# Kernel optimization log

Hardware: AMD Instinct MI355X
Metric: run time of the kernel (lower is better)

Reference implementation:

```python
import jax, jax.numpy as jnp
import numpy as np
from jax import lax

B, T, H, L, LAT, OUT, NH = 4096, 60, 512, 2, 128, 14, 4
EPS = 1e-5


def _ln(x, g, b):
    m = x.mean(-1, keepdims=True)
    v = ((x - m) ** 2).mean(-1, keepdims=True)
    return (x - m) / jnp.sqrt(v + EPS) * g + b


def setup_inputs() -> dict:
    key = jax.random.key(0)
    ks = jax.random.split(key, 24)
    f32 = jnp.float32
    def rn(k, shape, s=0.05):
        return jax.random.normal(k, shape, dtype=f32) * s
    return {
        'x': jax.random.normal(ks[0], (B, T, 17), dtype=f32),
        'conv1_w': rn(ks[1], (24, 9, 3)), 'conv1_b': rn(ks[2], (24,)),
        'bn1_g': jnp.ones(24, f32), 'bn1_b': jnp.zeros(24, f32),
        'bn1_rm': rn(ks[3], (24,), 0.1), 'bn1_rv': jnp.full((24,), 0.8, f32),
        'comp_w': rn(ks[4], (20, 8)), 'comp_b': rn(ks[5], (20,)),
        'proj_w': rn(ks[6], (H, 44)), 'proj_b': rn(ks[7], (H,)),
        'gates_w': rn(ks[8], (L, 5, H, 2 * H), 0.02), 'gates_b': rn(ks[9], (L, 5, H)),
        'retention': jnp.full((L, H), 0.9, f32),
        'expln_g': jnp.ones((L, H), f32), 'expln_b': jnp.zeros((L, H), f32),
        'ln_g': jnp.ones((L, H), f32), 'ln_b': jnp.zeros((L, H), f32),
        'attn_in_w': rn(ks[10], (3 * H, H), 0.02), 'attn_in_b': rn(ks[11], (3 * H,)),
        'attn_out_w': rn(ks[12], (H, H), 0.02), 'attn_out_b': rn(ks[13], (H,)),
        'bneck_w': rn(ks[14], (LAT, H)), 'bneck_b': rn(ks[15], (LAT,)),
        'bn2_g': jnp.ones(LAT, f32), 'bn2_b': jnp.zeros(LAT, f32),
        'bn2_rm': rn(ks[16], (LAT,), 0.1), 'bn2_rv': jnp.full((LAT,), 0.9, f32),
        'out_w': rn(ks[17], (OUT, LAT)), 'out_b': rn(ks[18], (OUT,)),
    }


def _forward(x, conv1_w, conv1_b, bn1_g, bn1_b, bn1_rm, bn1_rv, comp_w, comp_b,
             proj_w, proj_b, gates_w, gates_b, retention, expln_g, expln_b,
             ln_g, ln_b, attn_in_w, attn_in_b, attn_out_w, attn_out_b,
             bneck_w, bneck_b, bn2_g, bn2_b, bn2_rm, bn2_rv, out_w, out_b):
    bsz = x.shape[0]
    hd = proj_w.shape[0]
    nlayers = gates_w.shape[0]
    # --- conv branch on relative features (eval-mode BatchNorm) ---
    rel = x[:, :, :9].transpose(0, 2, 1)                      # [B,9,T]
    y = lax.conv_general_dilated(rel, conv1_w, (1,), [(1, 1)],
                                 dimension_numbers=('NCH', 'OIH', 'NCH'))
    y = jax.nn.relu(y + conv1_b[None, :, None])
    y = (y - bn1_rm[None, :, None]) / jnp.sqrt(bn1_rv + EPS)[None, :, None] \
        * bn1_g[None, :, None] + bn1_b[None, :, None]
    th = y.shape[2] // 2
    y = y[:, :, :th * 2].reshape(bsz, 24, th, 2).max(-1)      # MaxPool1d(2)
    rel_feat = y.transpose(0, 2, 1)                           # [B,30,24]
    # --- company embedding branch ---
    comp = jax.nn.relu(x[:, :30, 9:] @ comp_w.T + comp_b)     # [B,30,20]
    combined = jnp.concatenate([rel_feat, comp], -1) @ proj_w.T + proj_b  # [B,30,H]
    # --- stacked xLSTM over time ---
    h0 = jnp.zeros((nlayers, bsz, hd), x.dtype)
    c0 = jnp.zeros((nlayers, bsz, hd), x.dtype)
    def step(carry, x_t):
        h, c = carry
        inp = x_t
        hs, cs = [], []
        for l in range(nlayers):
            comb = jnp.concatenate([inp, h[l]], -1)           # [B,2H]
            g = jnp.einsum('bk,ghk->gbh', comb, gates_w[l]) + gates_b[l][:, None, :]
            f = jax.nn.sigmoid(g[0]); i = jax.nn.sigmoid(g[1])
            o = jax.nn.sigmoid(g[2]); cc = jnp.tanh(g[3]); m = jax.nn.sigmoid(g[4])
            r = retention[l]
            c_new = f * c[l] + i * cc
            c_new = c_new * r + (1 - r) * c[l]
            c_new = m * c_new + (1 - m) * c[l]
            o_exp = jax.nn.sigmoid(_ln(o, expln_g[l], expln_b[l]))  # exp(z)/(1+exp(z))
            h_new = _ln(o_exp * jnp.tanh(c_new), ln_g[l], ln_b[l])
            hs.append(h_new); cs.append(c_new)
            inp = h_new
        return (jnp.stack(hs), jnp.stack(cs)), inp
    _, seq = lax.scan(step, (h0, c0), combined.transpose(1, 0, 2))
    seq = seq.transpose(1, 0, 2)                              # [B,30,H]
    # --- multi-head self attention (eval, 4 heads) ---
    dh = hd // NH
    qkv = seq @ attn_in_w.T + attn_in_b
    q, k, v = jnp.split(qkv, 3, axis=-1)
    q = q.reshape(bsz, -1, NH, dh); k = k.reshape(bsz, -1, NH, dh); v = v.reshape(bsz, -1, NH, dh)
    scores = jnp.einsum('bqhd,bkhd->bhqk', q, k) / jnp.sqrt(jnp.float32(dh))
    attn = jnp.einsum('bhqk,bkhd->bqhd', jax.nn.softmax(scores, -1), v)
    attn = attn.reshape(bsz, -1, hd) @ attn_out_w.T + attn_out_b
    final = attn[:, -1, :]
    latent = final @ bneck_w.T + bneck_b
    latent = (latent - bn2_rm) / jnp.sqrt(bn2_rv + EPS) * bn2_g + bn2_b
    return latent @ out_w.T + out_b


def reference(x, conv1_w, conv1_b, bn1_g, bn1_b, bn1_rm, bn1_rv, comp_w, comp_b,
              proj_w, proj_b, gates_w, gates_b, retention, expln_g, expln_b,
              ln_g, ln_b, attn_in_w, attn_in_b, attn_out_w, attn_out_b,
              bneck_w, bneck_b, bn2_g, bn2_b, bn2_rm, bn2_rv, out_w, out_b):
    return _forward(x, conv1_w, conv1_b, bn1_g, bn1_b, bn1_rm, bn1_rv, comp_w, comp_b,
                    proj_w, proj_b, gates_w, gates_b, retention, expln_g, expln_b,
                    ln_g, ln_b, attn_in_w, attn_in_b, attn_out_w, attn_out_b,
                    bneck_w, bneck_b, bn2_g, bn2_b, bn2_rm, bn2_rv, out_w, out_b)
```

## Files before the change

kernel.cpp:

```cpp
#include <hip/hip_runtime.h>
#include <hip/hip_bf16.h>
#include <hip/hip_fp16.h>

#define B_   4096
#define T_   60
#define TT   30
#define H_   512
#define L_   2
#define NH_  4
#define DH_  128
#define LAT_ 128
#define OUT_ 14
#define NGATE_ (5*H_)
#define EPSF 1e-5f
#define FEATK 64
#define K0M  (FEATK + H_)

typedef __attribute__((ext_vector_type(8))) short bf16x8;
typedef __attribute__((ext_vector_type(4))) short sh4;
typedef __attribute__((ext_vector_type(4))) float f32x4;

__device__ __forceinline__ float sigmoidf_(float x) { return 1.0f / (1.0f + __expf(-x)); }
__device__ __forceinline__ float bf2f(short s) {
    return __uint_as_float(((unsigned)(unsigned short)s) << 16);
}

__device__ __forceinline__ void async_load16(const void* g, void* l) {
    __builtin_amdgcn_global_load_lds((const __attribute__((address_space(1))) void*)g,
                                     (__attribute__((address_space(3))) void*)l, 16, 0, 0);
}

__device__ __forceinline__ int perm_row(int n) {
    int g = n >> 9, j = n & 511;
    return (j >> 4) * 80 + g * 16 + (j & 15);
}

__global__ __launch_bounds__(256) void cvt_bf16(const float* __restrict__ in,
                                                __hip_bfloat16* __restrict__ out, long n) {
    long i = (long)blockIdx.x * blockDim.x + threadIdx.x;
    long stride = (long)gridDim.x * blockDim.x;
    for (; i < n; i += stride) out[i] = __float2bfloat16(in[i]);
}

__global__ __launch_bounds__(256) void zero_f32(float* __restrict__ p, long n) {
    long i = (long)blockIdx.x * blockDim.x + threadIdx.x;
    long stride = (long)gridDim.x * blockDim.x;
    for (; i < n; i += stride) p[i] = 0.0f;
}

__global__ __launch_bounds__(256)
void perm_w1(const float* __restrict__ gw, __hip_bfloat16* __restrict__ w1p) {
    long i = (long)blockIdx.x * 256 + threadIdx.x;
    if (i >= (long)NGATE_ * 2 * H_) return;
    int n = (int)(i >> 10), k = (int)(i & 1023);
    w1p[(long)perm_row(n) * (2 * H_) + k] = __float2bfloat16(gw[i]);
}

__global__ __launch_bounds__(256)
void build_w0m(const float* __restrict__ gw, const float* __restrict__ pw,
               const float* __restrict__ pb, const float* __restrict__ gb,
               __hip_bfloat16* __restrict__ w0p, float* __restrict__ bc) {
    const int tid = threadIdx.x;
    const int n = blockIdx.x * 4 + (tid >> 6);
    const int f = tid & 63;
    const long np = perm_row(n);
    const float* wrow = gw + (long)n * (2 * H_);
    float acc = 0.f;
    if (f < 44) {
        for (int k = 0; k < H_; ++k) acc += wrow[k] * pw[k * 44 + f];
    }
    w0p[np * K0M + f] = __float2bfloat16(acc);
    #pragma unroll
    for (int j = 0; j < 8; ++j) {
        int col = f * 8 + j;
        w0p[np * K0M + FEATK + col] = __float2bfloat16(wrow[H_ + col]);
    }
    float s = 0.f;
    #pragma unroll
    for (int j = 0; j < 8; ++j) s += wrow[f * 8 + j] * pb[f * 8 + j];
    #pragma unroll
    for (int off = 32; off > 0; off >>= 1) s += __shfl_down(s, off, 64);
    if (f == 0) bc[n] = gb[n] + s;
}

__global__ __launch_bounds__(256)
void build_wkt(const float* __restrict__ aiw, __hip_bfloat16* __restrict__ wkt) {
    int i = blockIdx.x * 256 + threadIdx.x;
    if (i >= 2048 * 128) return;
    int row = i >> 7;
    int k = i & 127;
    int h = row >> 9, j = row & 511;
    wkt[i] = __float2bfloat16(aiw[(H_ + h * 128 + k) * H_ + j]);
}

__global__ __launch_bounds__(256)
void frontend_kernel(const float* __restrict__ x,
                     const float* __restrict__ cw, const float* __restrict__ cb,
                     const float* __restrict__ bg, const float* __restrict__ bb,
                     const float* __restrict__ brm, const float* __restrict__ brv,
                     const float* __restrict__ compw, const float* __restrict__ compb,
                     __hip_bfloat16* __restrict__ feat_out) {
    const int b = blockIdx.x, tid = threadIdx.x;
    __shared__ float xs[T_ * 17];
    __shared__ float ybuf[24][T_];
    __shared__ float feat[TT][44];

    for (int i = tid; i < T_ * 17; i += 256) xs[i] = x[(long)b * T_ * 17 + i];
    __syncthreads();

    for (int i = tid; i < 24 * T_; i += 256) {
        int oc = i / T_, t = i % T_;
        float acc = cb[oc];
        #pragma unroll
        for (int kk = 0; kk < 3; ++kk) {
            int tt = t + kk - 1;
            if (tt >= 0 && tt < T_) {
                #pragma unroll
                for (int ic = 0; ic < 9; ++ic)
                    acc += xs[tt * 17 + ic] * cw[(oc * 9 + ic) * 3 + kk];
            }
        }
        acc = fmaxf(acc, 0.f);
        acc = (acc - brm[oc]) * rsqrtf(brv[oc] + EPSF) * bg[oc] + bb[oc];
        ybuf[oc][t] = acc;
    }
    __syncthreads();

    for (int i = tid; i < TT * 24; i += 256) {
        int u = i / 24, oc = i % 24;
        feat[u][oc] = fmaxf(ybuf[oc][2 * u], ybuf[oc][2 * u + 1]);
    }
    for (int i = tid; i < TT * 20; i += 256) {
        int u = i / 20, oc = i % 20;
        float acc = compb[oc];
        #pragma unroll
        for (int j = 0; j < 8; ++j) acc += xs[u * 17 + 9 + j] * compw[oc * 8 + j];
        feat[u][24 + oc] = fmaxf(acc, 0.f);
    }
    __syncthreads();

    for (int i = tid; i < TT * FEATK; i += 256) {
        int u = i >> 6, c = i & 63;
        float v = (c < 44) ? feat[u][c] : 0.f;
        feat_out[((long)b * TT + u) * FEATK + c] = __float2bfloat16(v);
    }
}

template <int WRITE_BF16>
__device__ __forceinline__
void gemm_core(const __hip_bfloat16* __restrict__ A0, int lda0,
               const __hip_bfloat16* __restrict__ A1, int lda1, int ksplit,
               const __hip_bfloat16* __restrict__ W, int ldw,
               const float* __restrict__ bias,
               void* __restrict__ Cout, int ldc, int K, int bx, int by) {
    __shared__ __hip_bfloat16 As[128 * 64];
    __shared__ __hip_bfloat16 Bs[128 * 64];
    const int tid = threadIdx.x;
    const int wave = tid >> 6, lane = tid & 63;
    const long m0 = (long)by * 128;
    const long n0 = (long)bx * 128;

    f32x4 acc[4][4] = {};

    for (int k0 = 0; k0 < K; k0 += 64) {
        __syncthreads();
        #pragma unroll
        for (int it = 0; it < 4; ++it) {
            int id = it * 256 + tid;
            int row = id >> 3;
            int kc = ((id & 7) ^ (row & 7)) << 3;
            int gk = k0 + kc;
            const __hip_bfloat16* srcA;
            if (gk < ksplit) srcA = A0 + (m0 + row) * (long)lda0 + gk;
            else             srcA = A1 + (m0 + row) * (long)lda1 + (gk - ksplit);
            async_load16(srcA, &As[id * 8]);
            const __hip_bfloat16* srcB = W + (n0 + row) * (long)ldw + gk;
            async_load16(srcB, &Bs[id * 8]);
        }
        __syncthreads();
        #pragma unroll
        for (int ks = 0; ks < 2; ++ks) {
            const int kb = ((ks * 4 + (lane >> 4)) ^ (lane & 7)) << 3;
            const int ar = (wave >> 1) * 64 + (lane & 15);
            const int br = (wave & 1) * 64 + (lane & 15);
            bf16x8 afr[4], bfr[4];
            #pragma unroll
            for (int i = 0; i < 4; ++i) afr[i] = *(const bf16x8*)&As[(ar + i * 16) * 64 + kb];
            #pragma unroll
            for (int i = 0; i < 4; ++i) bfr[i] = *(const bf16x8*)&Bs[(br + i * 16) * 64 + kb];
            #pragma unroll
            for (int mi = 0; mi < 4; ++mi)
                #pragma unroll
                for (int ni = 0; ni < 4; ++ni)
                    acc[mi][ni] = __builtin_amdgcn_mfma_f32_16x16x32_bf16(afr[mi], bfr[ni], acc[mi][ni], 0, 0, 0);
        }
    }

    const int cr = (lane >> 4) * 4;
    const int ccol = lane & 15;
    #pragma unroll
    for (int ni = 0; ni < 4; ++ni) {
        long col = n0 + (wave & 1) * 64 + ni * 16 + ccol;
        float bv = bias ? bias[col] : 0.f;
        #pragma unroll
        for (int mi = 0; mi < 4; ++mi) {
            long rowb = m0 + (wave >> 1) * 64 + mi * 16 + cr;
            #pragma unroll
            for (int r = 0; r < 4; ++r) {
                float v = acc[mi][ni][r] + bv;
                if (WRITE_BF16)
                    ((__hip_bfloat16*)Cout)[(rowb + r) * (long)ldc + col] = __float2bfloat16(v);
                else
                    ((float*)Cout)[(rowb + r) * (long)ldc + col] = v;
            }
        }
    }
}

template <int WRITE_BF16>
__global__ __launch_bounds__(256)
void gemm_bias(const __hip_bfloat16* __restrict__ A0, int lda0,
               const __hip_bfloat16* __restrict__ A1, int lda1, int ksplit,
               const __hip_bfloat16* __restrict__ W, int ldw,
               const float* __restrict__ bias,
               void* __restrict__ Cout, int ldc, int K) {
    gemm_core<WRITE_BF16>(A0, lda0, A1, lda1, ksplit, W, ldw, bias, Cout, ldc, K,
                          blockIdx.x, blockIdx.y);
}

__device__ __forceinline__
void fused_gate_core(const __hip_bfloat16* __restrict__ A0, int lda0,
                     const __hip_bfloat16* __restrict__ A1, int lda1,
                     int ksplit, int K,
                     const __hip_bfloat16* __restrict__ Wp, int ldw,
                     const float* __restrict__ bias,
                     const float* __restrict__ ret,
                     float* __restrict__ c_t,
                     __half* __restrict__ opre,
                     __half* __restrict__ tcn,
                     int m, int nblk) {
    __shared__ __hip_bfloat16 As[2][128 * 64];
    __shared__ __hip_bfloat16 Bs[2][80 * 64];
    const int tid = threadIdx.x;
    const int wave = tid >> 6, lane = tid & 63;
    const long m0 = (long)m * 128;
    const int n0row = nblk * 80;
    const int jbase = nblk * 16;
    const int rsel = lane & 15;
    const int q = lane >> 4;

    const int kc = ((tid & 7) ^ ((tid >> 3) & 7)) << 3;
    const int srow = tid >> 3;
    const __hip_bfloat16* pA0_t = A0 + (m0 + srow) * (long)lda0 + kc;
    const __hip_bfloat16* pA1_t =
        A1 ? (A1 + (m0 + srow) * (long)lda1 + kc - ksplit) : pA0_t;
    const __hip_bfloat16* pB_t = Wp + (long)(n0row + srow) * ldw + kc;
    const int ks_slab = ksplit >> 6;
    const int nslab = K >> 6;

    auto stage = [&](int hb, int kk) {
        const long koff = (long)kk << 6;
        const __hip_bfloat16* pa;
        long la;
        if (kk < ks_slab) { pa = pA0_t; la = lda0; }
        else              { pa = pA1_t; la = lda1; }
        #pragma unroll
        for (int it = 0; it < 4; ++it)
            async_load16(pa + (long)it * 32 * la + koff,
                         &As[hb][it * 2048 + tid * 8]);
        #pragma unroll
        for (int it = 0; it < 2; ++it)
            async_load16(pB_t + (long)it * 32 * ldw + koff,
                         &Bs[hb][it * 2048 + tid * 8]);
        if (tid < 128)
            async_load16(pB_t + (long)64 * ldw + koff,
                         &Bs[hb][4096 + tid * 8]);
    };

    stage(0, 0);
    f32x4 acc[2][5] = {};

    for (int kk = 0; kk < nslab; ++kk) {
        const int hb = kk & 1;
        __syncthreads();
        if (kk + 1 < nslab) stage(hb ^ 1, kk + 1);
        #pragma unroll
        for (int ks = 0; ks < 2; ++ks) {
            const int kb = ((ks * 4 + q) ^ (lane & 7)) << 3;
            bf16x8 afr[2], bfr[5];
            #pragma unroll
            for (int i = 0; i < 2; ++i)
                afr[i] = *(const bf16x8*)&As[hb][(wave * 32 + i * 16 + rsel) * 64 + kb];
            #pragma unroll
            for (int i = 0; i < 5; ++i)
                bfr[i] = *(const bf16x8*)&Bs[hb][(i * 16 + rsel) * 64 + kb];
            #pragma unroll
            for (int mi = 0; mi < 2; ++mi)
                #pragma unroll
                for (int ni = 0; ni < 5; ++ni)
                    acc[mi][ni] = __builtin_amdgcn_mfma_f32_16x16x32_bf16(bfr[ni], afr[mi], acc[mi][ni], 0, 0, 0);
        }
    }

    #pragma unroll
    for (int mi = 0; mi < 2; ++mi) {
        const long b = m0 + wave * 32 + mi * 16 + rsel;
        sh4 ov, tv;
        #pragma unroll
        for (int r = 0; r < 4; ++r) {
            const int jg = jbase + 4 * q + r;
            float f  = sigmoidf_(acc[mi][0][r] + bias[jg]);
            float ii = sigmoidf_(acc[mi][1][r] + bias[512 + jg]);
            float o  = sigmoidf_(acc[mi][2][r] + bias[1024 + jg]);
            float cc = tanhf(acc[mi][3][r] + bias[1536 + jg]);
            float mg = sigmoidf_(acc[mi][4][r] + bias[2048 + jg]);
            float cold = c_t[(long)jg * B_ + b];
            float rr = ret[jg];
            float cn = f * cold + ii * cc;
            cn = cn * rr + (1.f - rr) * cold;
            cn = mg * cn + (1.f - mg) * cold;
            c_t[(long)jg * B_ + b] = cn;
            __half oh = __float2half(o);
            __half th = __float2half(tanhf(cn));
            ov[r] = *(short*)&oh;
            tv[r] = *(short*)&th;
        }
        *(sh4*)&opre[b * H_ + jbase + 4 * q] = ov;
        *(sh4*)&tcn [b * H_ + jbase + 4 * q] = tv;
    }
}

__global__ __launch_bounds__(256)
void fused_gate_single(const __hip_bfloat16* A0, int lda0, const __hip_bfloat16* A1,
                       int lda1, int ksplit, int K,
                       const __hip_bfloat16* Wp, int ldw,
                       const float* bias, const float* ret, float* c_t,
                       __half* opre, __half* tcn) {
    const int id = blockIdx.x;
    const int xcd = id & 7;
    const int rest = id >> 3;
    const int m = xcd * 4 + (rest & 3);
    const int n = (rest >> 2) & 31;
    fused_gate_core(A0, lda0, A1, lda1, ksplit, K, Wp, ldw, bias, ret, c_t,
                    opre, tcn, m, n);
}

__global__ __launch_bounds__(256)
void fused_gate_dual(const __hip_bfloat16* A0a, int lda0a, const __hip_bfloat16* A1a,
                     int lda1a, int ksplita, int Ka,
                     const __hip_bfloat16* Wpa, int ldwa,
                     const float* biasa, const float* reta, float* cta,
                     __half* oprea, __half* tcna,
                     const __hip_bfloat16* A0b, int lda0b, const __hip_bfloat16* A1b,
                     int lda1b, int ksplitb, int Kb,
                     const __hip_bfloat16* Wpb, int ldwb,
                     const float* biasb, const float* retb, float* ctb,
                     __half* opreb, __half* tcnb) {
    const int id = blockIdx.x;
    const int xcd = id & 7;
    const int rest = id >> 3;
    const int m = xcd * 4 + (rest & 3);
    const int n = (rest >> 2) & 31;
    const int z = rest >> 7;
    if (z == 0)
        fused_gate_core(A0a, lda0a, A1a, lda1a, ksplita, Ka, Wpa, ldwa,
                        biasa, reta, cta, oprea, tcna, m, n);
    else
        fused_gate_core(A0b, lda0b, A1b, lda1b, ksplitb, Kb, Wpb, ldwb,
                        biasb, retb, ctb, opreb, tcnb, m, n);
}

__device__ __forceinline__ void block_reduce2(float& a, float& b, float* red) {
    #pragma unroll
    for (int off = 32; off > 0; off >>= 1) {
        a += __shfl_down(a, off, 64);
        b += __shfl_down(b, off, 64);
    }
    int lane = threadIdx.x & 63, w = threadIdx.x >> 6;
    if (lane == 0) { red[w] = a; red[8 + w] = b; }
    __syncthreads();
    a = red[0] + red[1] + red[2] + red[3];
    b = red[8] + red[9] + red[10] + red[11];
    __syncthreads();
}

__device__ __forceinline__
void gate_ln_body(const __half* __restrict__ opre,
                  const __half* __restrict__ tcn,
                  const float* __restrict__ elg, const float* __restrict__ elb,
                  const float* __restrict__ lng, const float* __restrict__ lnb,
                  __hip_bfloat16* __restrict__ hout, long hstride, int b) {
    const int tid = threadIdx.x;
    __shared__ float red[16];

    float o_[2], t_[2];
    float s = 0.f, s2 = 0.f;
    #pragma unroll
    for (int u = 0; u < 2; ++u) {
        int j = tid + u * 256;
        float o = __half2float(opre[(long)b * H_ + j]);
        float t = __half2float(tcn[(long)b * H_ + j]);
        o_[u] = o; t_[u] = t;
        s += o; s2 += o * o;
    }
    block_reduce2(s, s2, red);
    float mean = s * (1.f / H_);
    float var = s2 * (1.f / H_) - mean * mean;
    float rstd = rsqrtf(var + EPSF);

    float val[2];
    float s3 = 0.f, s4 = 0.f;
    #pragma unroll
    for (int u = 0; u < 2; ++u) {
        int j = tid + u * 256;
        float on = (o_[u] - mean) * rstd * elg[j] + elb[j];
        float v = sigmoidf_(on) * t_[u];
        val[u] = v; s3 += v; s4 += v * v;
    }
    block_reduce2(s3, s4, red);
    float mean2 = s3 * (1.f / H_);
    float var2 = s4 * (1.f / H_) - mean2 * mean2;
    float rstd2 = rsqrtf(var2 + EPSF);
    #pragma unroll
    for (int u = 0; u < 2; ++u) {
        int j = tid + u * 256;
        float h = (val[u] - mean2) * rstd2 * lng[j] + lnb[j];
        hout[(long)b * hstride + j] = __float2bfloat16(h);
    }
}

__global__ __launch_bounds__(256)
void gate_ln(const __half* __restrict__ opre,
             const __half* __restrict__ tcn,
             const float* __restrict__ elg, const float* __restrict__ elb,
             const float* __restrict__ lng, const float* __restrict__ lnb,
             __hip_bfloat16* __restrict__ hout, long hstride) {
    gate_ln_body(opre, tcn, elg, elb, lng, lnb, hout, hstride, blockIdx.x);
}

__global__ __launch_bounds__(256)
void gate_ln_dual(const __half* oa, const __half* ta,
                  const float* elga, const float* elba,
                  const float* lnga, const float* lnba,
                  __hip_bfloat16* houta, long hstridea,
                  const __half* ob, const __half* tb,
                  const float* elgb, const float* elbb,
                  const float* lngb, const float* lnbb,
                  __hip_bfloat16* houtb, long hstrideb) {
    int bid = blockIdx.x;
    bool isB = bid >= B_;
    int b = isB ? bid - B_ : bid;
    gate_ln_body(isB ? ob : oa, isB ? tb : ta,
                 isB ? elgb : elga, isB ? elbb : elba,
                 isB ? lngb : lnga, isB ? lnbb : lnba,
                 isB ? houtb : houta, isB ? hstrideb : hstridea, b);
}

__global__ __launch_bounds__(256)
void attn_fused(const __hip_bfloat16* __restrict__ seq,
                const __hip_bfloat16* __restrict__ U,
                __hip_bfloat16* __restrict__ sbar) {
    const int b = blockIdx.x, tid = threadIdx.x;
    const int h = tid >> 6, lane = tid & 63;
    const int c0 = lane * 8;
    __shared__ __hip_bfloat16 ss[TT * H_];
    __shared__ float ps[NH_ * TT];
    __shared__ float we[NH_ * TT];
    const float scale = 0.08838834764831845f;

    const __hip_bfloat16* srow = seq + (size_t)b * TT * H_;
    for (int i = tid; i < TT * H_ / 8; i += 256)
        async_load16(srow + i * 8, &ss[i * 8]);

    float uq[8];
    {
        bf16x8 uv = *(const bf16x8*)&U[(size_t)b * (NH_ * H_) + h * H_ + c0];
        for (int j = 0; j < 8; ++j) uq[j] = bf2f(uv[j]);
    }
    __syncthreads();

    for (int t = 0; t < TT; ++t) {
        bf16x8 sv = *(const bf16x8*)&ss[t * H_ + c0];
        float a = 0.f;
        for (int j = 0; j < 8; ++j) a += uq[j] * bf2f(sv[j]);
        a += __shfl_xor(a, 32);
        a += __shfl_xor(a, 16);
        a += __shfl_xor(a, 8);
        a += __shfl_xor(a, 4);
        a += __shfl_xor(a, 2);
        a += __shfl_xor(a, 1);
        if (lane == 0) ps[h * TT + t] = a * scale;
    }
    __syncthreads();

    float mx = -1e30f;
    for (int t = 0; t < TT; ++t) mx = fmaxf(mx, ps[h * TT + t]);
    float den = 0.f;
    for (int t = 0; t < TT; ++t) den += __expf(ps[h * TT + t] - mx);
    float inv = 1.f / den;
    if (lane < TT) we[h * TT + lane] = __expf(ps[h * TT + lane] - mx) * inv;
    __syncthreads();

    float accv[8];
    for (int j = 0; j < 8; ++j) accv[j] = 0.f;
    for (int t = 0; t < TT; ++t) {
        float w = we[h * TT + t];
        bf16x8 sv = *(const bf16x8*)&ss[t * H_ + c0];
        for (int j = 0; j < 8; ++j) accv[j] += w * bf2f(sv[j]);
    }
    bf16x8 outv;
    for (int j = 0; j < 8; ++j) {
        __hip_bfloat16 hv = __float2bfloat16(accv[j]);
        outv[j] = *(short*)&hv;
    }
    *(bf16x8*)&sbar[(size_t)b * (NH_ * H_) + h * H_ + c0] = outv;
}

__global__ __launch_bounds__(128)
void head_kernel(const float* __restrict__ lat_in,
                 const float* __restrict__ g2, const float* __restrict__ b2,
                 const float* __restrict__ rm2, const float* __restrict__ rv2,
                 const float* __restrict__ ow, const float* __restrict__ ob,
                 float* __restrict__ out) {
    const int b = blockIdx.x, tid = threadIdx.x;
    __shared__ float ls[LAT_];
    float a = lat_in[(long)b * LAT_ + tid];
    ls[tid] = (a - rm2[tid]) * rsqrtf(rv2[tid] + EPSF) * g2[tid] + b2[tid];
    __syncthreads();
    if (tid < OUT_) {
        float acc = ob[tid];
        #pragma unroll 4
        for (int j = 0; j < LAT_; ++j) acc += ls[j] * ow[tid * LAT_ + j];
        out[(long)b * OUT_ + tid] = acc;
    }
}

extern "C" void kernel_launch(void* const* d_in, const int* in_sizes, int n_in,
                              void* d_out, int out_size, void* d_ws, size_t ws_size,
                              hipStream_t stream) {
    const float* x        = (const float*)d_in[0];
    const float* conv1_w  = (const float*)d_in[1];
    const float* conv1_b  = (const float*)d_in[2];
    const float* bn1_g    = (const float*)d_in[3];
    const float* bn1_b    = (const float*)d_in[4];
    const float* bn1_rm   = (const float*)d_in[5];
    const float* bn1_rv   = (const float*)d_in[6];
    const float* comp_w   = (const float*)d_in[7];
    const float* comp_b   = (const float*)d_in[8];
    const float* proj_w   = (const float*)d_in[9];
    const float* proj_b   = (const float*)d_in[10];
    const float* gates_w  = (const float*)d_in[11];
    const float* gates_b  = (const float*)d_in[12];
    const float* retention= (const float*)d_in[13];
    const float* expln_g  = (const float*)d_in[14];
    const float* expln_b  = (const float*)d_in[15];
    const float* ln_g     = (const float*)d_in[16];
    const float* ln_b     = (const float*)d_in[17];
    const float* attn_in_w  = (const float*)d_in[18];
    const float* attn_in_b  = (const float*)d_in[19];
    const float* attn_out_w = (const float*)d_in[20];
    const float* attn_out_b = (const float*)d_in[21];
    const float* bneck_w  = (const float*)d_in[22];
    const float* bneck_b  = (const float*)d_in[23];
    const float* bn2_g    = (const float*)d_in[24];
    const float* bn2_b    = (const float*)d_in[25];
    const float* bn2_rm   = (const float*)d_in[26];
    const float* bn2_rv   = (const float*)d_in[27];
    const float* out_w    = (const float*)d_in[28];
    const float* out_b    = (const float*)d_in[29];
    float* out = (float*)d_out;

    char* base = (char*)d_ws;
    size_t off = 0;
    auto alloc = [&](size_t nbytes) -> char* {
        char* p = base + off;
        off += (nbytes + 255) & ~(size_t)255;
        return p;
    };
    __hip_bfloat16* seq_bf = (__hip_bfloat16*)alloc((size_t)B_ * TT * H_ * 2);
    size_t g_bytes = (size_t)B_ * NGATE_ * 2;
    char* un = alloc(2 * g_bytes);
    __half* opreA = (__half*)un;
    __half* tcnA  = (__half*)(un + (size_t)4 * 1024 * 1024);
    __half* opreB = (__half*)(un + (size_t)8 * 1024 * 1024);
    __half* tcnB  = (__half*)(un + (size_t)12 * 1024 * 1024);
    __hip_bfloat16* U_bf    = (__hip_bfloat16*)un;
    __hip_bfloat16* sbar_bf = (__hip_bfloat16*)(un + (size_t)16 * 1024 * 1024);
    __hip_bfloat16* wkt_bf  = (__hip_bfloat16*)(un + (size_t)32 * 1024 * 1024);
    __hip_bfloat16* wv_bf   = (__hip_bfloat16*)(un + (size_t)35 * 1024 * 1024);
    __hip_bfloat16* feat_bf = (__hip_bfloat16*)alloc((size_t)B_ * TT * FEATK * 2);
    float*          c0t   = (float*)alloc((size_t)B_ * H_ * 4);
    float*          c1t   = (float*)alloc((size_t)B_ * H_ * 4);
    __hip_bfloat16* h0_bf = (__hip_bfloat16*)alloc((size_t)B_ * H_ * 2);
    __hip_bfloat16* q_bf  = (__hip_bfloat16*)alloc((size_t)B_ * H_ * 2);
    __hip_bfloat16* fin_bf = q_bf;
    __hip_bfloat16* av_bf = (__hip_bfloat16*)alloc((size_t)B_ * H_ * 2);
    float*          lat_f = (float*)alloc((size_t)B_ * LAT_ * 4);
    __hip_bfloat16* w1p_bf = (__hip_bfloat16*)alloc((size_t)NGATE_ * 2 * H_ * 2);
    __hip_bfloat16* w0p_bf = (__hip_bfloat16*)alloc((size_t)NGATE_ * K0M * 2);
    float*          bc_f  = (float*)alloc((size_t)NGATE_ * 4);
    __hip_bfloat16* ai_bf = (__hip_bfloat16*)alloc((size_t)H_ * H_ * 2);
    __hip_bfloat16* ao_bf = (__hip_bfloat16*)alloc((size_t)H_ * H_ * 2);
    __hip_bfloat16* bw_bf = (__hip_bfloat16*)alloc((size_t)LAT_ * H_ * 2);
    (void)ws_size; (void)in_sizes; (void)n_in; (void)out_size;

    const int WL = 5 * H_ * 2 * H_;
    perm_w1<<<(NGATE_ * 2 * H_) / 256, 256, 0, stream>>>(gates_w + WL, w1p_bf);
    build_w0m<<<NGATE_ / 4, 256, 0, stream>>>(gates_w, proj_w, proj_b, gates_b,
                                              w0p_bf, bc_f);
    cvt_bf16<<<256, 256, 0, stream>>>(attn_in_w, ai_bf, (long)H_ * H_);
    cvt_bf16<<<256, 256, 0, stream>>>(attn_out_w, ao_bf, (long)H_ * H_);
    cvt_bf16<<<64, 256, 0, stream>>>(bneck_w, bw_bf, (long)LAT_ * H_);
    zero_f32<<<2048, 256, 0, stream>>>(c0t, (long)2 * B_ * H_);

    frontend_kernel<<<B_, 256, 0, stream>>>(x, conv1_w, conv1_b, bn1_g, bn1_b, bn1_rm,
                                            bn1_rv, comp_w, comp_b, feat_bf);

    fused_gate_single<<<1024, 256, 0, stream>>>(
        feat_bf, TT * FEATK, (const __hip_bfloat16*)nullptr, 0, FEATK, FEATK,
        w0p_bf, K0M, bc_f, retention, c0t, opreB, tcnB);
    gate_ln<<<B_, 256, 0, stream>>>(opreB, tcnB, expln_g, expln_b,
                                    ln_g, ln_b, h0_bf, H_);

    for (int t = 0; t < TT - 1; ++t) {
        fused_gate_dual<<<2048, 256, 0, stream>>>(
            h0_bf, H_, (t == 0) ? (const __hip_bfloat16*)nullptr
                                : seq_bf + (size_t)(t - 1) * H_,
            TT * H_, H_, (t == 0) ? H_ : 2 * H_,
            w1p_bf, 2 * H_, gates_b + NGATE_, retention + H_, c1t, opreA, tcnA,
            feat_bf + (size_t)(t + 1) * FEATK, TT * FEATK, h0_bf, H_, FEATK, K0M,
            w0p_bf, K0M, bc_f, retention, c0t, opreB, tcnB);
        gate_ln_dual<<<2 * B_, 256, 0, stream>>>(
            opreA, tcnA, expln_g + H_, expln_b + H_, ln_g + H_, ln_b + H_,
            seq_bf + (size_t)t * H_, TT * H_,
            opreB, tcnB, expln_g, expln_b, ln_g, ln_b, h0_bf, H_);
    }
    fused_gate_single<<<1024, 256, 0, stream>>>(
        h0_bf, H_, seq_bf + (size_t)(TT - 2) * H_, TT * H_, H_, 2 * H_,
        w1p_bf, 2 * H_, gates_b + NGATE_, retention + H_, c1t, opreA, tcnA);
    gate_ln<<<B_, 256, 0, stream>>>(opreA, tcnA, expln_g + H_, expln_b + H_,
                                    ln_g + H_, ln_b + H_,
                                    seq_bf + (size_t)(TT - 1) * H_, TT * H_);

    build_wkt<<<1024, 256, 0, stream>>>(attn_in_w, wkt_bf);
    cvt_bf16<<<1024, 256, 0, stream>>>(attn_in_w + (size_t)(2 * H_) * H_, wv_bf,
                                       (long)H_ * H_);

    gemm_bias<1><<<dim3(H_ / 128, B_ / 128), 256, 0, stream>>>(
        seq_bf + (size_t)29 * H_, TT * H_, (const __hip_bfloat16*)nullptr, 0, H_,
        ai_bf, H_, attn_in_b, (void*)q_bf, H_, H_);

    for (int h = 0; h < NH_; ++h)
        gemm_bias<1><<<dim3(4, B_ / 128), 256, 0, stream>>>(
            q_bf + h * DH_, H_, (const __hip_bfloat16*)nullptr, 0, DH_,
            wkt_bf + (size_t)h * 512 * DH_, DH_, (const float*)nullptr,
            (void*)(U_bf + h * 512), 2048, DH_);

    attn_fused<<<B_, 256, 0, stream>>>(seq_bf, U_bf, sbar_bf);

    for (int h = 0; h < NH_; ++h)
        gemm_bias<1><<<dim3(1, B_ / 128), 256, 0, stream>>>(
            sbar_bf + h * 512, 2048, (const __hip_bfloat16*)nullptr, 0, H_,
            wv_bf + (size_t)h * DH_ * H_, H_, attn_in_b + 2 * H_ + h * DH_,
            (void*)(av_bf + h * DH_), H_, H_);

    gemm_bias<1><<<dim3(H_ / 128, B_ / 128), 256, 0, stream>>>(
        av_bf, H_, (const __hip_bfloat16*)nullptr, 0, H_,
        ao_bf, H_, attn_out_b, (void*)fin_bf, H_, H_);

    gemm_bias<0><<<dim3(LAT_ / 128, B_ / 128), 256, 0, stream>>>(
        fin_bf, H_, (const __hip_bfloat16*)nullptr, 0, H_,
        bw_bf, H_, bneck_b, (void*)lat_f, LAT_, H_);
    head_kernel<<<B_, 128, 0, stream>>>(lat_f, bn2_g, bn2_b, bn2_rm, bn2_rv,
                                        out_w, out_b, out);
}
```

Measured before the change: 2.439 ms.

## Load A fragments directly into registers and stage weights in four-slab LDS chunks

The fused gate GEMM no longer stages the activation tile through shared memory. Each wave now loads its own A fragments straight from global memory into registers, prefetching one slab ahead. Weight tiles are staged into four LDS slots and refilled in chunks of four slabs, so there are fewer barriers per slab. The aim is to cut LDS traffic and synchronisation. The cost is that A loads are uncoalesced per-lane 16-byte reads. Weight staging is also no longer overlapped with compute, because each next chunk is loaded only after a barrier.

New measurement: 2.933 ms. 20.2% more time.

```diff
diff --git a/kernel.cpp b/kernel.cpp
--- a/kernel.cpp
+++ b/kernel.cpp
@@ -239,8 +239,7 @@
                      __half* __restrict__ opre,
                      __half* __restrict__ tcn,
                      int m, int nblk) {
-    __shared__ __hip_bfloat16 As[2][128 * 64];
-    __shared__ __hip_bfloat16 Bs[2][80 * 64];
+    __shared__ __hip_bfloat16 Ws[4][80 * 64];
     const int tid = threadIdx.x;
     const int wave = tid >> 6, lane = tid & 63;
     const long m0 = (long)m * 128;
@@ -251,54 +250,83 @@
 
     const int kc = ((tid & 7) ^ ((tid >> 3) & 7)) << 3;
     const int srow = tid >> 3;
-    const __hip_bfloat16* pA0_t = A0 + (m0 + srow) * (long)lda0 + kc;
-    const __hip_bfloat16* pA1_t =
-        A1 ? (A1 + (m0 + srow) * (long)lda1 + kc - ksplit) : pA0_t;
     const __hip_bfloat16* pB_t = Wp + (long)(n0row + srow) * ldw + kc;
+
+    const long arow = m0 + wave * 32 + rsel;
+    const __hip_bfloat16* pa0 = A0 + arow * (long)lda0 + q * 8;
+    const __hip_bfloat16* pa1 =
+        A1 ? (A1 + arow * (long)lda1 + q * 8 - ksplit) : pa0;
+    const long a0s16 = (long)16 * lda0;
+    const long a1s16 = (long)16 * lda1;
+
     const int ks_slab = ksplit >> 6;
     const int nslab = K >> 6;
-
-    auto stage = [&](int hb, int kk) {
+    const int nchunk = (nslab + 3) >> 2;
+
+    auto stageW = [&](int slot, int kk) {
         const long koff = (long)kk << 6;
-        const __hip_bfloat16* pa;
-        long la;
-        if (kk < ks_slab) { pa = pA0_t; la = lda0; }
-        else              { pa = pA1_t; la = lda1; }
-        #pragma unroll
-        for (int it = 0; it < 4; ++it)
-            async_load16(pa + (long)it * 32 * la + koff,
-                         &As[hb][it * 2048 + tid * 8]);
         #pragma unroll
         for (int it = 0; it < 2; ++it)
             async_load16(pB_t + (long)it * 32 * ldw + koff,
-                         &Bs[hb][it * 2048 + tid * 8]);
+                         &Ws[slot][it * 2048 + tid * 8]);
         if (tid < 128)
             async_load16(pB_t + (long)64 * ldw + koff,
-                         &Bs[hb][4096 + tid * 8]);
+                         &Ws[slot][4096 + tid * 8]);
     };
-
-    stage(0, 0);
+    auto loadA = [&](int kk, bf16x8 (&dst)[2][2]) {
+        const __hip_bfloat16* pa;
+        long as16;
+        if (kk < ks_slab) { pa = pa0 + ((long)kk << 6); as16 = a0s16; }
+        else              { pa = pa1 + ((long)kk << 6); as16 = a1s16; }
+        #pragma unroll
+        for (int mi = 0; mi < 2; ++mi)
+            #pragma unroll
+            for (int ks = 0; ks < 2; ++ks)
+                dst[mi][ks] = *(const bf16x8*)(pa + mi * as16 + ks * 32);
+    };
+
+    {
+        int send = nslab < 4 ? nslab : 4;
+        for (int s = 0; s < send; ++s) stageW(s, s);
+    }
+    bf16x8 aCur[2][2], aNxt[2][2];
+    loadA(0, aCur);
     f32x4 acc[2][5] = {};
 
-    for (int kk = 0; kk < nslab; ++kk) {
-        const int hb = kk & 1;
+    for (int c = 0; c < nchunk; ++c) {
         __syncthreads();
-        if (kk + 1 < nslab) stage(hb ^ 1, kk + 1);
-        #pragma unroll
-        for (int ks = 0; ks < 2; ++ks) {
-            const int kb = ((ks * 4 + q) ^ (lane & 7)) << 3;
-            bf16x8 afr[2], bfr[5];
+        const int sbeg = c * 4;
+        const int send = (sbeg + 4 < nslab) ? sbeg + 4 : nslab;
+        for (int kk = sbeg; kk < send; ++kk) {
+            const bool more = (kk + 1 < nslab);
+            if (more) loadA(kk + 1, aNxt);
+            const int slot = kk & 3;
             #pragma unroll
-            for (int i = 0; i < 2; ++i)
-                afr[i] = *(const bf16x8*)&As[hb][(wave * 32 + i * 16 + rsel) * 64 + kb];
-            #pragma unroll
-            for (int i = 0; i < 5; ++i)
-                bfr[i] = *(const bf16x8*)&Bs[hb][(i * 16 + rsel) * 64 + kb];
-            #pragma unroll
-            for (int mi = 0; mi < 2; ++mi)
+            for (int ks = 0; ks < 2; ++ks) {
+                const int kb = ((ks * 4 + q) ^ (lane & 7)) << 3;
+                bf16x8 bfr[5];
                 #pragma unroll
-                for (int ni = 0; ni < 5; ++ni)
-                    acc[mi][ni] = __builtin_amdgcn_mfma_f32_16x16x32_bf16(bfr[ni], afr[mi], acc[mi][ni], 0, 0, 0);
+                for (int i = 0; i < 5; ++i)
+                    bfr[i] = *(const bf16x8*)&Ws[slot][(i * 16 + rsel) * 64 + kb];
+                #pragma unroll
+                for (int mi = 0; mi < 2; ++mi)
+                    #pragma unroll
+                    for (int ni = 0; ni < 5; ++ni)
+                        acc[mi][ni] = __builtin_amdgcn_mfma_f32_16x16x32_bf16(bfr[ni], aCur[mi][ks], acc[mi][ni], 0, 0, 0);
+            }
+            if (more) {
+                #pragma unroll
+                for (int mi = 0; mi < 2; ++mi)
+                    #pragma unroll
+                    for (int ks = 0; ks < 2; ++ks)
+                        aCur[mi][ks] = aNxt[mi][ks];
+            }
+        }
+        __syncthreads();
+        if (c + 1 < nchunk) {
+            const int nbeg = (c + 1) * 4;
+            const int nend = (nbeg + 4 < nslab) ? nbeg + 4 : nslab;
+            for (int kk = nbeg; kk < nend; ++kk) stageW(kk & 3, kk);
         }
     }
 
```
